# Performance work log

Measured on AMD Instinct MI355X. Metric: run time of the kernel, lower is better.

Reference implementation:

```python
import jax, jax.numpy as jnp
import numpy as np

N_NODES = 65536
N_EDGES = 524288
N_GRAPHS = 512
G_NODES = 10000
NUM_DISEASES = 2000
IN_DIM = 128
HID = 256  # 2 * IN_DIM (z_emb concat feat)
D_FEAT = 512
C_FEAT = 512
MAX_Z = 4000


def setup_inputs() -> dict:
    key = jax.random.key(0)
    ks = jax.random.split(key, 20)
    rn = lambda k, shape: jax.random.normal(k, shape, dtype=jnp.float32) * 0.05
    return {
        "z": jax.random.randint(ks[0], (N_NODES,), 0, MAX_Z),
        "node_id": jnp.sort(jax.random.randint(ks[1], (N_NODES,), 0, G_NODES)),
        "src": jax.random.randint(ks[2], (N_EDGES,), 0, N_NODES),
        "dst": jax.random.randint(ks[3], (N_EDGES,), 0, N_NODES),
        "graph_ids": jnp.sort(jax.random.randint(ks[4], (N_NODES,), 0, N_GRAPHS)),
        "z_table": rn(ks[5], (MAX_Z, IN_DIM)),
        "d_feat_tab": rn(ks[6], (G_NODES, D_FEAT)),
        "c_feat_tab": rn(ks[7], (G_NODES, C_FEAT)),
        "Wd": rn(ks[8], (D_FEAT, IN_DIM)),
        "Wc": rn(ks[9], (C_FEAT, IN_DIM)),
        "gin_W1": rn(ks[10], (HID, HID)), "gin_b1": jnp.zeros((HID,), jnp.float32),
        "gin_W2": rn(ks[11], (HID, HID)), "gin_b2": jnp.zeros((HID,), jnp.float32),
        "sage_Wself": rn(ks[12], (HID, HID)),
        "sage_Wneigh": rn(ks[13], (HID, HID)),
        "sage_b": jnp.zeros((HID,), jnp.float32),
        "lin1_W": rn(ks[14], (HID, HID)), "lin1_b": jnp.zeros((HID,), jnp.float32),
        "lin2_W": rn(ks[15], (HID, 1)), "lin2_b": jnp.zeros((1,), jnp.float32),
    }


def reference(z, node_id, src, dst, graph_ids, z_table, d_feat_tab, c_feat_tab,
              Wd, Wc, gin_W1, gin_b1, gin_W2, gin_b2,
              sage_Wself, sage_Wneigh, sage_b, lin1_W, lin1_b, lin2_W, lin2_b):
    # --- input feature construction (Model.forward) ---
    z_emb = z_table[z]                               # [N, IN_DIM]
    d_proj = d_feat_tab[node_id] @ Wd                # d_fc (bias=False)
    c_proj = c_feat_tab[node_id] @ Wc                # c_fc (bias=False)
    disease = (node_id <= NUM_DISEASES)[:, None]
    # node_id is sorted -> masked concat order == node order
    feat = jnp.where(disease, d_proj, c_proj)        # [N, IN_DIM]
    x = jnp.concatenate([z_emb, feat], axis=1)       # [N, HID]
    # --- GINConv: sum aggregation, eps=0, mlp = Lin->ReLU->Lin ---
    agg = jax.ops.segment_sum(x[src], dst, num_segments=N_NODES)
    h = x + agg
    h = jax.nn.relu(h @ gin_W1 + gin_b1) @ gin_W2 + gin_b2
    # --- SAGEConv('mean'): fc_self(h) + fc_neigh(mean_neighbors) + bias ---
    deg = jax.ops.segment_sum(jnp.ones((N_EDGES,), h.dtype), dst, num_segments=N_NODES)
    mean_n = jax.ops.segment_sum(h[src], dst, num_segments=N_NODES) / jnp.maximum(deg, 1.0)[:, None]
    h = h @ sage_Wself + mean_n @ sage_Wneigh + sage_b
    # --- per-graph max pooling readout ---
    g = jax.ops.segment_max(h, graph_ids, num_segments=N_GRAPHS, indices_are_sorted=True)
    g = jnp.where(jnp.isfinite(g), g, 0.0)           # guard empty graphs
    # --- head: Linear -> ReLU -> (dropout p=0, eval) -> Linear ---
    h = jax.nn.relu(g @ lin1_W + lin1_b)
    return h @ lin2_W + lin2_b                       # [N_GRAPHS, 1]
```

## Files before the change

kernel.cpp:

```cpp
#include <hip/hip_runtime.h>
#include <hip/hip_bf16.h>

#define N_NODES     65536
#define N_EDGES     524288
#define N_GRAPHS    512
#define G_NODES_N   10000
#define NUM_DIS     2000
#define IN_DIM      128
#define HID         256
#define D_FEAT      512
#define MAX_Z       4000

typedef _Float16 half8 __attribute__((ext_vector_type(8)));
typedef float    f32x4 __attribute__((ext_vector_type(4)));

typedef __attribute__((address_space(1))) const void as1_void;
typedef __attribute__((address_space(3))) void       as3_void;

__global__ __launch_bounds__(256) void prep_kernel(
    const float* __restrict__ Ws, const float* __restrict__ Wn,
    const float* __restrict__ Wd, const float* __restrict__ Wc,
    const float* __restrict__ W1, const float* __restrict__ W2,
    const float* __restrict__ z_table,
    const int* __restrict__ z, const int* __restrict__ node_id,
    _Float16* __restrict__ WsT, _Float16* __restrict__ WnT,
    _Float16* __restrict__ WdT, _Float16* __restrict__ WcT,
    _Float16* __restrict__ W12P, _Float16* __restrict__ zt16,
    int2* __restrict__ zn2, int* __restrict__ cnt, int* __restrict__ flags)
{
    const int b = blockIdx.x;
    const int tid = threadIdx.x;
    if (b < 64) {
        __shared__ float tile[64][65];
        const float* W; _Float16* T; int K, N, k0, n0;
        if (b < 32) {
            const int mat = b >> 4, t = b & 15;
            K = HID; N = HID; k0 = (t >> 2) * 64; n0 = (t & 3) * 64;
            W = (mat == 0) ? Ws : Wn;
            T = (mat == 0) ? WsT : WnT;
        } else {
            const int bb = b - 32;
            const int mat = bb >> 4, t = bb & 15;
            K = D_FEAT; N = IN_DIM; k0 = (t >> 1) * 64; n0 = (t & 1) * 64;
            W = (mat == 0) ? Wd : Wc;
            T = (mat == 0) ? WdT : WcT;
        }
        const int tx = tid & 63, ty = tid >> 6;
        #pragma unroll
        for (int r = 0; r < 64; r += 4)
            tile[r + ty][tx] = W[(size_t)(k0 + r + ty) * N + n0 + tx];
        __syncthreads();
        #pragma unroll
        for (int c = 0; c < 64; c += 4)
            T[(size_t)(n0 + c + ty) * K + k0 + tx] = (_Float16)tile[tx][c + ty];
    } else if (b < 576) {
        const int bb = b - 64;
        const int mat = bb >> 8;
        const int k = bb & 255;
        const int n = tid;
        const float* W = mat ? W2 : W1;
        const float v = W[(size_t)k * HID + n];
        const size_t idx = (size_t)(mat * 8 + (k >> 5)) * 8192
                         + (size_t)((((k >> 3) & 3) * 256 + n) * 8 + (k & 7));
        W12P[idx] = (_Float16)v;
    } else if (b < 826) {
        const size_t base = ((size_t)(b - 576) * 256 + tid) * 8;
        const float4 f0 = *(const float4*)(z_table + base);
        const float4 f1 = *(const float4*)(z_table + base + 4);
        half8 h;
        h[0]=(_Float16)f0.x; h[1]=(_Float16)f0.y; h[2]=(_Float16)f0.z; h[3]=(_Float16)f0.w;
        h[4]=(_Float16)f1.x; h[5]=(_Float16)f1.y; h[6]=(_Float16)f1.z; h[7]=(_Float16)f1.w;
        *(half8*)(zt16 + base) = h;
    } else if (b < 890) {
        const int base = (b - 826) * 1024 + tid * 4;
        *(int4*)(cnt + base) = make_int4(0, 0, 0, 0);
        if (b == 826 && tid < 128) flags[tid] = 0;
    } else {
        const int i = (b - 890) * 256 + tid;
        zn2[i] = make_int2(z[i], node_id[i]);
    }
}

__global__ __launch_bounds__(256) void proj_hist_kernel(
    const float* __restrict__ dtab, const float* __restrict__ ctab,
    const _Float16* __restrict__ WdT, const _Float16* __restrict__ WcT,
    _Float16* __restrict__ proj,
    const int* __restrict__ dst, int* __restrict__ cnt)
{
    const int blk = blockIdx.x;
    if (blk >= 79) {
        const int e = (blk - 79) * 256 + threadIdx.x;
        if (e < N_EDGES) atomicAdd(&cnt[dst[e]], 1);
        return;
    }
    __shared__ _Float16 Alds[128 * 40];
    __shared__ _Float16 Blds[128 * 40];
    const float* tab; const _Float16* WT; int base, M, bm;
    if (blk < 16) { tab = dtab; WT = WdT; base = 0;           M = NUM_DIS + 1;             bm = blk * 128; }
    else          { tab = ctab; WT = WcT; base = NUM_DIS + 1; M = G_NODES_N - NUM_DIS - 1; bm = (blk - 16) * 128; }
    const int tid  = threadIdx.x;
    const int wave = tid >> 6, lane = tid & 63;
    const int q    = lane >> 4, l16 = lane & 15;
    const int mbase = (wave & 1) * 64, nbase = (wave >> 1) * 64;
    const int r = tid >> 1, s = tid & 1;

    f32x4 acc[4][4] = {};

    for (int kc = 0; kc < 16; ++kc) {
        const int k0 = kc * 32;
        const int arow = min(bm + r, M - 1);
        const float* gA = tab + (size_t)(base + arow) * D_FEAT + k0 + s * 16;
        const _Float16* gB = WT + (size_t)r * D_FEAT + k0 + s * 16;
        const float4 f0 = ((const float4*)gA)[0];
        const float4 f1 = ((const float4*)gA)[1];
        const float4 f2 = ((const float4*)gA)[2];
        const float4 f3 = ((const float4*)gA)[3];
        const half8 hb0 = *(const half8*)gB;
        const half8 hb1 = *(const half8*)(gB + 8);
        half8 h0, h1;
        h0[0]=(_Float16)f0.x; h0[1]=(_Float16)f0.y; h0[2]=(_Float16)f0.z; h0[3]=(_Float16)f0.w;
        h0[4]=(_Float16)f1.x; h0[5]=(_Float16)f1.y; h0[6]=(_Float16)f1.z; h0[7]=(_Float16)f1.w;
        h1[0]=(_Float16)f2.x; h1[1]=(_Float16)f2.y; h1[2]=(_Float16)f2.z; h1[3]=(_Float16)f2.w;
        h1[4]=(_Float16)f3.x; h1[5]=(_Float16)f3.y; h1[6]=(_Float16)f3.z; h1[7]=(_Float16)f3.w;
        __syncthreads();
        *(half8*)&Alds[r * 40 + s * 16]     = h0;
        *(half8*)&Alds[r * 40 + s * 16 + 8] = h1;
        *(half8*)&Blds[r * 40 + s * 16]     = hb0;
        *(half8*)&Blds[r * 40 + s * 16 + 8] = hb1;
        __syncthreads();
        half8 a[4], b[4];
        #pragma unroll
        for (int i = 0; i < 4; ++i)
            a[i] = *(const half8*)&Alds[(mbase + i * 16 + l16) * 40 + q * 8];
        #pragma unroll
        for (int j = 0; j < 4; ++j)
            b[j] = *(const half8*)&Blds[(nbase + j * 16 + l16) * 40 + q * 8];
        #pragma unroll
        for (int i = 0; i < 4; ++i)
            #pragma unroll
            for (int j = 0; j < 4; ++j)
                acc[i][j] = __builtin_amdgcn_mfma_f32_16x16x32_f16(a[i], b[j], acc[i][j], 0, 0, 0);
    }

    #pragma unroll
    for (int j = 0; j < 4; ++j) {
        const int colg = nbase + j * 16 + l16;
        #pragma unroll
        for (int i = 0; i < 4; ++i) {
            #pragma unroll
            for (int rr = 0; rr < 4; ++rr) {
                const int row = bm + mbase + i * 16 + q * 4 + rr;
                if (row < M)
                    proj[(size_t)(base + row) * IN_DIM + colg] = (_Float16)acc[i][j][rr];
            }
        }
    }
}

__global__ __launch_bounds__(256) void scan_fused_kernel(
    const int* __restrict__ cnt, int* __restrict__ row_ptr,
    int* __restrict__ fill, int* __restrict__ flags)
{
    __shared__ int a[256], b[256];
    __shared__ int sums[64];
    __shared__ int segbase;
    const int t = threadIdx.x;
    const int blk = blockIdx.x;
    const int base = blk * 1024 + t * 4;
    const int4 c = *(const int4*)(cnt + base);
    const int s = c.x + c.y + c.z + c.w;
    a[t] = s;
    __syncthreads();
    int* in = a; int* out = b;
    for (int off = 1; off < 256; off <<= 1) {
        out[t] = in[t] + ((t >= off) ? in[t - off] : 0);
        __syncthreads();
        int* tmp = in; in = out; out = tmp;
    }
    if (t == 0) {
        atomicExch(&flags[64 + blk], in[255]);
        __threadfence();
        atomicAdd(&flags[0], 1);
        while (atomicAdd(&flags[0], 0) < 64) {}
    }
    __syncthreads();
    if (t < 64) sums[t] = atomicAdd(&flags[64 + t], 0);
    __syncthreads();
    if (t == 0) {
        int pfx = 0;
        for (int i = 0; i < blk; ++i) pfx += sums[i];
        segbase = pfx;
        if (blk == 63) {
            int tot = pfx;
            for (int i = blk; i < 64; ++i) tot += sums[i];
            row_ptr[N_NODES] = tot;
        }
    }
    __syncthreads();
    const int run = in[t] - s + segbase;
    int4 r;
    r.x = run; r.y = run + c.x; r.z = r.y + c.y; r.w = r.z + c.z;
    *(int4*)(row_ptr + base) = r;
    *(int4*)(fill + base) = r;
}

__global__ __launch_bounds__(256) void scatter_kernel(
    const int* __restrict__ src, const int* __restrict__ dst,
    const int2* __restrict__ zn2,
    int* __restrict__ fill, int* __restrict__ col, int2* __restrict__ colzn)
{
    const int e = blockIdx.x * 256 + threadIdx.x;
    if (e < N_EDGES) {
        const int s = src[e];
        const int pos = atomicAdd(&fill[dst[e]], 1);
        col[pos] = s;
        colzn[pos] = zn2[s];
    }
}

__global__ __launch_bounds__(256) void gin_fused_kernel(
    const int* __restrict__ row_ptr, const int2* __restrict__ colzn,
    const int2* __restrict__ zn2,
    const _Float16* __restrict__ zt16, const _Float16* __restrict__ proj,
    const _Float16* __restrict__ W12P,
    const float* __restrict__ b1, const float* __restrict__ b2,
    _Float16* __restrict__ H)
{
    __shared__ _Float16 Apanel[64 * 264];
    __shared__ _Float16 Blds[8192];

    const int bm   = blockIdx.x * 64;
    const int tid  = threadIdx.x;
    const int wave = tid >> 6, lane = tid & 63;
    const int q    = lane >> 4, l16 = lane & 15;
    const int nbase = wave * 64;
    const int sb   = wave * 256 + lane;

    {
        #pragma unroll
        for (int tt = 0; tt < 4; ++tt) {
            const int seg = (wave * 4 + tt) * 64 + lane;
            __builtin_amdgcn_global_load_lds((as1_void*)(W12P + seg * 8),
                (as3_void*)&Blds[(wave * 4 + tt) * 64 * 8], 16, 0, 0);
        }
    }

    {
        const int p = tid & 7;
        #pragma unroll 1
        for (int pass = 0; pass < 2; ++pass) {
            const int r  = (tid >> 3) + (pass << 5);
            const int gr = bm + r;
            const int beg = row_ptr[gr], end = row_ptr[gr + 1];
            float za[16], pa[16];
            {
                const int2 zn = zn2[gr];
                const half8* zp = (const half8*)(zt16 + (size_t)zn.x * IN_DIM + p * 16);
                const half8* pp = (const half8*)(proj + (size_t)zn.y * IN_DIM + p * 16);
                const half8 z0 = zp[0], z1 = zp[1], p0 = pp[0], p1 = pp[1];
                #pragma unroll
                for (int i = 0; i < 8; ++i) {
                    za[i] = (float)z0[i]; za[8 + i] = (float)z1[i];
                    pa[i] = (float)p0[i]; pa[8 + i] = (float)p1[i];
                }
            }
            int e = beg;
            for (; e + 4 <= end; e += 4) {
                const int2 znA = colzn[e],     znB = colzn[e + 1];
                const int2 znC = colzn[e + 2], znD = colzn[e + 3];
                const half8* zpA = (const half8*)(zt16 + (size_t)znA.x * IN_DIM + p * 16);
                const half8* ppA = (const half8*)(proj + (size_t)znA.y * IN_DIM + p * 16);
                const half8* zpB = (const half8*)(zt16 + (size_t)znB.x * IN_DIM + p * 16);
                const half8* ppB = (const half8*)(proj + (size_t)znB.y * IN_DIM + p * 16);
                const half8* zpC = (const half8*)(zt16 + (size_t)znC.x * IN_DIM + p * 16);
                const half8* ppC = (const half8*)(proj + (size_t)znC.y * IN_DIM + p * 16);
                const half8* zpD = (const half8*)(zt16 + (size_t)znD.x * IN_DIM + p * 16);
                const half8* ppD = (const half8*)(proj + (size_t)znD.y * IN_DIM + p * 16);
                const half8 zA0 = zpA[0], zA1 = zpA[1], pA0 = ppA[0], pA1 = ppA[1];
                const half8 zB0 = zpB[0], zB1 = zpB[1], pB0 = ppB[0], pB1 = ppB[1];
                const half8 zC0 = zpC[0], zC1 = zpC[1], pC0 = ppC[0], pC1 = ppC[1];
                const half8 zD0 = zpD[0], zD1 = zpD[1], pD0 = ppD[0], pD1 = ppD[1];
                #pragma unroll
                for (int i = 0; i < 8; ++i) {
                    za[i]     += ((float)zA0[i] + (float)zB0[i]) + ((float)zC0[i] + (float)zD0[i]);
                    za[8 + i] += ((float)zA1[i] + (float)zB1[i]) + ((float)zC1[i] + (float)zD1[i]);
                    pa[i]     += ((float)pA0[i] + (float)pB0[i]) + ((float)pC0[i] + (float)pD0[i]);
                    pa[8 + i] += ((float)pA1[i] + (float)pB1[i]) + ((float)pC1[i] + (float)pD1[i]);
                }
            }
            for (; e + 2 <= end; e += 2) {
                const int2 znA = colzn[e];
                const int2 znB = colzn[e + 1];
                const half8* zpA = (const half8*)(zt16 + (size_t)znA.x * IN_DIM + p * 16);
                const half8* ppA = (const half8*)(proj + (size_t)znA.y * IN_DIM + p * 16);
                const half8* zpB = (const half8*)(zt16 + (size_t)znB.x * IN_DIM + p * 16);
                const half8* ppB = (const half8*)(proj + (size_t)znB.y * IN_DIM + p * 16);
                const half8 zA0 = zpA[0], zA1 = zpA[1], pA0 = ppA[0], pA1 = ppA[1];
                const half8 zB0 = zpB[0], zB1 = zpB[1], pB0 = ppB[0], pB1 = ppB[1];
                #pragma unroll
                for (int i = 0; i < 8; ++i) {
                    za[i]     += (float)zA0[i] + (float)zB0[i];
                    za[8 + i] += (float)zA1[i] + (float)zB1[i];
                    pa[i]     += (float)pA0[i] + (float)pB0[i];
                    pa[8 + i] += (float)pA1[i] + (float)pB1[i];
                }
            }
            if (e < end) {
                const int2 zn = colzn[e];
                const half8* zp = (const half8*)(zt16 + (size_t)zn.x * IN_DIM + p * 16);
                const half8* pp = (const half8*)(proj + (size_t)zn.y * IN_DIM + p * 16);
                const half8 z0 = zp[0], z1 = zp[1], p0 = pp[0], p1 = pp[1];
                #pragma unroll
                for (int i = 0; i < 8; ++i) {
                    za[i] += (float)z0[i]; za[8 + i] += (float)z1[i];
                    pa[i] += (float)p0[i]; pa[8 + i] += (float)p1[i];
                }
            }
            half8 oz0, oz1, op0, op1;
            #pragma unroll
            for (int i = 0; i < 8; ++i) {
                oz0[i] = (_Float16)za[i];     oz1[i] = (_Float16)za[8 + i];
                op0[i] = (_Float16)pa[i];     op1[i] = (_Float16)pa[8 + i];
            }
            *(half8*)&Apanel[r * 264 + p * 16]           = oz0;
            *(half8*)&Apanel[r * 264 + p * 16 + 8]       = oz1;
            *(half8*)&Apanel[r * 264 + 128 + p * 16]     = op0;
            *(half8*)&Apanel[r * 264 + 128 + p * 16 + 8] = op1;
        }
    }
    __syncthreads();

    half8 pf0, pf1, pf2, pf3;
    auto pfetch = [&](int c) {
        const _Float16* s = W12P + (size_t)c * 8192 + (size_t)sb * 8;
        pf0 = *(const half8*)(s);
        pf1 = *(const half8*)(s + 512);
        pf2 = *(const half8*)(s + 1024);
        pf3 = *(const half8*)(s + 1536);
    };
    pfetch(1);

    f32x4 acc[4][4] = {};
    for (int c = 0; c < 16; ++c) {
        const int kl = (c & 7) * 32;
        half8 a[4], b[4];
        #pragma unroll
        for (int i = 0; i < 4; ++i)
            a[i] = *(const half8*)&Apanel[(i * 16 + l16) * 264 + kl + q * 8];
        #pragma unroll
        for (int j = 0; j < 4; ++j)
            b[j] = *(const half8*)&Blds[(q * 256 + nbase + j * 16 + l16) * 8];
        #pragma unroll
        for (int i = 0; i < 4; ++i)
            #pragma unroll
            for (int j = 0; j < 4; ++j)
                acc[i][j] = __builtin_amdgcn_mfma_f32_16x16x32_f16(a[i], b[j], acc[i][j], 0, 0, 0);
        if (c == 15) break;
        __syncthreads();
        *(half8*)&Blds[sb * 8]         = pf0;
        *(half8*)&Blds[(sb + 64) * 8]  = pf1;
        *(half8*)&Blds[(sb + 128) * 8] = pf2;
        *(half8*)&Blds[(sb + 192) * 8] = pf3;
        if (c == 7) {
            #pragma unroll
            for (int j = 0; j < 4; ++j) {
                const int colg = nbase + j * 16 + l16;
                const float bv = b1[colg];
                #pragma unroll
                for (int i = 0; i < 4; ++i)
                    #pragma unroll
                    for (int rr = 0; rr < 4; ++rr) {
                        const float v = fmaxf(acc[i][j][rr] + bv, 0.0f);
                        Apanel[(i * 16 + q * 4 + rr) * 264 + colg] = (_Float16)v;
                        acc[i][j][rr] = 0.0f;
                    }
            }
        }
        if (c < 14) pfetch(c + 2);
        __syncthreads();
    }

    #pragma unroll
    for (int j = 0; j < 4; ++j) {
        const int colg = nbase + j * 16 + l16;
        const float bv = b2[colg];
        #pragma unroll
        for (int i = 0; i < 4; ++i)
            #pragma unroll
            for (int rr = 0; rr < 4; ++rr) {
                const int rowg = bm + i * 16 + q * 4 + rr;
                H[(size_t)rowg * HID + colg] = (_Float16)(acc[i][j][rr] + bv);
            }
    }
}

__global__ __launch_bounds__(256) void csr_agg_kernel(
    const int* __restrict__ row_ptr, const int* __restrict__ col,
    const _Float16* __restrict__ F, _Float16* __restrict__ OUT)
{
    const int t = blockIdx.x * 256 + threadIdx.x;
    const int d = t >> 5;
    const int q = t & 31;
    const int beg = row_ptr[d];
    const int end = row_ptr[d + 1];
    float acc[8] = {0.f,0.f,0.f,0.f,0.f,0.f,0.f,0.f};
    int e = beg;
    for (; e + 8 <= end; e += 8) {
        const int s0 = col[e],     s1 = col[e + 1];
        const int s2 = col[e + 2], s3 = col[e + 3];
        const int s4 = col[e + 4], s5 = col[e + 5];
        const int s6 = col[e + 6], s7 = col[e + 7];
        const half8 v0 = *(const half8*)(F + (size_t)s0 * HID + q * 8);
        const half8 v1 = *(const half8*)(F + (size_t)s1 * HID + q * 8);
        const half8 v2 = *(const half8*)(F + (size_t)s2 * HID + q * 8);
        const half8 v3 = *(const half8*)(F + (size_t)s3 * HID + q * 8);
        const half8 v4 = *(const half8*)(F + (size_t)s4 * HID + q * 8);
        const half8 v5 = *(const half8*)(F + (size_t)s5 * HID + q * 8);
        const half8 v6 = *(const half8*)(F + (size_t)s6 * HID + q * 8);
        const half8 v7 = *(const half8*)(F + (size_t)s7 * HID + q * 8);
        #pragma unroll
        for (int i = 0; i < 8; ++i)
            acc[i] += (((float)v0[i] + (float)v1[i]) + ((float)v2[i] + (float)v3[i]))
                    + (((float)v4[i] + (float)v5[i]) + ((float)v6[i] + (float)v7[i]));
    }
    for (; e + 4 <= end; e += 4) {
        const int s0 = col[e],     s1 = col[e + 1];
        const int s2 = col[e + 2], s3 = col[e + 3];
        const half8 v0 = *(const half8*)(F + (size_t)s0 * HID + q * 8);
        const half8 v1 = *(const half8*)(F + (size_t)s1 * HID + q * 8);
        const half8 v2 = *(const half8*)(F + (size_t)s2 * HID + q * 8);
        const half8 v3 = *(const half8*)(F + (size_t)s3 * HID + q * 8);
        #pragma unroll
        for (int i = 0; i < 8; ++i)
            acc[i] += ((float)v0[i] + (float)v1[i]) + ((float)v2[i] + (float)v3[i]);
    }
    for (; e < end; ++e) {
        const half8 v0 = *(const half8*)(F + (size_t)col[e] * HID + q * 8);
        #pragma unroll
        for (int i = 0; i < 8; ++i) acc[i] += (float)v0[i];
    }
    const float rs = 1.0f / fmaxf((float)(end - beg), 1.0f);
    half8 o;
    #pragma unroll
    for (int i = 0; i < 8; ++i) o[i] = (_Float16)(acc[i] * rs);
    *(half8*)(OUT + (size_t)d * HID + q * 8) = o;
}

__global__ __launch_bounds__(256) void mfma_gemm_kernel(
    const _Float16* __restrict__ A1, const _Float16* __restrict__ A2,
    const _Float16* __restrict__ B1T, const _Float16* __restrict__ B2T,
    const float* __restrict__ bias, _Float16* __restrict__ Ch)
{
    __shared__ _Float16 Alds[128 * 32];
    __shared__ _Float16 Blds[128 * 32];
    const int bm   = blockIdx.x * 128;
    const int bn   = blockIdx.y * 128;
    const int tid  = threadIdx.x;
    const int wave = tid >> 6, lane = tid & 63;
    const int q    = lane >> 4, l16 = lane & 15;
    const int mbase = (wave & 1) * 64, nbase = (wave >> 1) * 64;

    const int i0 = wave * 128 + lane;
    const int i1 = i0 + 64;
    const int r0 = i0 >> 2, s0 = i0 & 3;
    const int r1 = i1 >> 2, s1 = i1 & 3;

    half8 pa0, pa1, pb0, pb1;
    auto pfetch = [&](int kc) {
        const int k0 = (kc & 7) * 32;
        const _Float16* Ab = (kc < 8) ? A1 : A2;
        const _Float16* Bb = (kc < 8) ? B1T : B2T;
        pa0 = *(const half8*)(Ab + (size_t)(bm + r0) * HID + k0 + s0 * 8);
        pa1 = *(const half8*)(Ab + (size_t)(bm + r1) * HID + k0 + s1 * 8);
        pb0 = *(const half8*)(Bb + (size_t)(bn + r0) * HID + k0 + s0 * 8);
        pb1 = *(const half8*)(Bb + (size_t)(bn + r1) * HID + k0 + s1 * 8);
    };
    pfetch(0);

    f32x4 acc[4][4] = {};

    for (int kc = 0; kc < 16; ++kc) {
        __syncthreads();
        *(half8*)&Alds[i0 * 8] = pa0;
        *(half8*)&Alds[i1 * 8] = pa1;
        *(half8*)&Blds[i0 * 8] = pb0;
        *(half8*)&Blds[i1 * 8] = pb1;
        if (kc < 15) pfetch(kc + 1);
        __syncthreads();
        half8 a[4], b[4];
        #pragma unroll
        for (int i = 0; i < 4; ++i)
            a[i] = *(const half8*)&Alds[(mbase + i * 16 + l16) * 32 + q * 8];
        #pragma unroll
        for (int j = 0; j < 4; ++j)
            b[j] = *(const half8*)&Blds[(nbase + j * 16 + l16) * 32 + q * 8];
        #pragma unroll
        for (int i = 0; i < 4; ++i)
            #pragma unroll
            for (int j = 0; j < 4; ++j)
                acc[i][j] = __builtin_amdgcn_mfma_f32_16x16x32_f16(a[i], b[j], acc[i][j], 0, 0, 0);
    }

    #pragma unroll
    for (int j = 0; j < 4; ++j) {
        const int colg = bn + nbase + j * 16 + l16;
        const float bv = bias[colg];
        #pragma unroll
        for (int i = 0; i < 4; ++i) {
            #pragma unroll
            for (int rr = 0; rr < 4; ++rr) {
                const int rowg = bm + mbase + i * 16 + q * 4 + rr;
                Ch[(size_t)rowg * HID + colg] = (_Float16)(acc[i][j][rr] + bv);
            }
        }
    }
}

__global__ __launch_bounds__(256) void pool_head_kernel(
    const _Float16* __restrict__ H2, const int* __restrict__ gid,
    const float* __restrict__ W1, const float* __restrict__ b1,
    const float* __restrict__ W2, const float* __restrict__ b2,
    float* __restrict__ out)
{
    const int g = blockIdx.x;
    const int tid = threadIdx.x;
    int lo = 0, hi = N_NODES;
    while (lo < hi) { const int mid = (lo + hi) >> 1; if (gid[mid] < g) lo = mid + 1; else hi = mid; }
    const int start = lo;
    hi = N_NODES;
    while (lo < hi) { const int mid = (lo + hi) >> 1; if (gid[mid] < g + 1) lo = mid + 1; else hi = mid; }
    const int end = lo;

    const int rowofs = tid >> 5;
    const int q = tid & 31;
    float m8[8];
    #pragma unroll
    for (int k = 0; k < 8; ++k) m8[k] = -INFINITY;
    for (int i = start + rowofs; i < end; i += 8) {
        const half8 v = *(const half8*)(H2 + (size_t)i * HID + q * 8);
        #pragma unroll
        for (int k = 0; k < 8; ++k) m8[k] = fmaxf(m8[k], (float)v[k]);
    }
    __shared__ float part[8][256];
    #pragma unroll
    for (int k = 0; k < 8; ++k) part[rowofs][q * 8 + k] = m8[k];
    __syncthreads();
    __shared__ float row[HID];
    __shared__ float red[HID];
    const int j = tid;
    float m = part[0][j];
    #pragma unroll
    for (int r = 1; r < 8; ++r) m = fmaxf(m, part[r][j]);
    row[j] = (m == -INFINITY) ? 0.0f : m;
    __syncthreads();
    float acc = b1[j];
    #pragma unroll 8
    for (int k = 0; k < HID; ++k)
        acc = fmaf(row[k], W1[k * HID + j], acc);
    acc = fmaxf(acc, 0.f);
    red[j] = acc * W2[j];
    __syncthreads();
    for (int s = 128; s > 0; s >>= 1) {
        if (j < s) red[j] += red[j + s];
        __syncthreads();
    }
    if (j == 0) out[g] = red[0] + b2[0];
}

extern "C" void kernel_launch(void* const* d_in, const int* in_sizes, int n_in,
                              void* d_out, int out_size, void* d_ws, size_t ws_size,
                              hipStream_t stream)
{
    const int*   z         = (const int*)d_in[0];
    const int*   node_id   = (const int*)d_in[1];
    const int*   src       = (const int*)d_in[2];
    const int*   dst       = (const int*)d_in[3];
    const int*   graph_ids = (const int*)d_in[4];
    const float* z_table   = (const float*)d_in[5];
    const float* d_feat    = (const float*)d_in[6];
    const float* c_feat    = (const float*)d_in[7];
    const float* Wd        = (const float*)d_in[8];
    const float* Wc        = (const float*)d_in[9];
    const float* gin_W1    = (const float*)d_in[10];
    const float* gin_b1    = (const float*)d_in[11];
    const float* gin_W2    = (const float*)d_in[12];
    const float* gin_b2    = (const float*)d_in[13];
    const float* sage_Wself  = (const float*)d_in[14];
    const float* sage_Wneigh = (const float*)d_in[15];
    const float* sage_b    = (const float*)d_in[16];
    const float* lin1_W    = (const float*)d_in[17];
    const float* lin1_b    = (const float*)d_in[18];
    const float* lin2_W    = (const float*)d_in[19];
    const float* lin2_b    = (const float*)d_in[20];
    float* out = (float*)d_out;

    const size_t NH = (size_t)N_NODES * HID;
    char* wsb = (char*)d_ws;
    _Float16* Hh   = (_Float16*)wsb;                     wsb += NH * 2;
    _Float16* AGGh = (_Float16*)wsb;                     wsb += NH * 2;
    _Float16* H2h  = (_Float16*)wsb;                     wsb += NH * 2;
    _Float16* projh= (_Float16*)wsb;                     wsb += (size_t)G_NODES_N * IN_DIM * 2;
    _Float16* W12P = (_Float16*)wsb;                     wsb += 16 * 8192 * 2;
    _Float16* WsT  = (_Float16*)wsb;                     wsb += HID * HID * 2;
    _Float16* WnT  = (_Float16*)wsb;                     wsb += HID * HID * 2;
    _Float16* WdT  = (_Float16*)wsb;                     wsb += D_FEAT * IN_DIM * 2;
    _Float16* WcT  = (_Float16*)wsb;                     wsb += D_FEAT * IN_DIM * 2;
    _Float16* zt16 = (_Float16*)wsb;                     wsb += (size_t)MAX_Z * IN_DIM * 2;
    int2* zn2      = (int2*)wsb;                         wsb += (size_t)N_NODES * 8;
    int2* colzn    = (int2*)wsb;                         wsb += (size_t)N_EDGES * 8;
    int* row_ptr   = (int*)wsb;                          wsb += (N_NODES + 4) * 4;
    int* cnt       = (int*)wsb;                          wsb += N_NODES * 4;
    int* fill      = (int*)wsb;                          wsb += N_NODES * 4;
    int* col       = (int*)wsb;                          wsb += N_EDGES * 4;
    int* flags     = (int*)wsb;                          wsb += 128 * 4;

    prep_kernel<<<1146, 256, 0, stream>>>(
        sage_Wself, sage_Wneigh, Wd, Wc, gin_W1, gin_W2, z_table, z, node_id,
        WsT, WnT, WdT, WcT, W12P, zt16, zn2, cnt, flags);

    proj_hist_kernel<<<79 + N_EDGES / 256, 256, 0, stream>>>(
        d_feat, c_feat, WdT, WcT, projh, dst, cnt);

    scan_fused_kernel<<<64, 256, 0, stream>>>(cnt, row_ptr, fill, flags);
    scatter_kernel<<<N_EDGES / 256, 256, 0, stream>>>(src, dst, zn2, fill, col, colzn);

    gin_fused_kernel<<<N_NODES / 64, 256, 0, stream>>>(
        row_ptr, colzn, zn2, zt16, projh, W12P, gin_b1, gin_b2, Hh);

    csr_agg_kernel<<<(N_NODES * 32) / 256, 256, 0, stream>>>(row_ptr, col, Hh, AGGh);

    dim3 ggrid(N_NODES / 128, HID / 128);
    mfma_gemm_kernel<<<ggrid, 256, 0, stream>>>(Hh, AGGh, WsT, WnT, sage_b, H2h);

    pool_head_kernel<<<N_GRAPHS, 256, 0, stream>>>(
        H2h, graph_ids, lin1_W, lin1_b, lin2_W, lin2_b, out);
}
```

Baseline: 343.9 us.

## Use 512-thread blocks in fused GIN kernel with pre-scaled byte offsets

The fused GIN kernel now launches 512 threads per block, so each thread gathers one row instead of two sequential passes. The 8 waves are arranged as a 2x4 grid over the 64x256 output tile, which halves each wave's MFMA accumulator footprint. zn2 indices are pre-shifted to byte offsets to drop address multiplies, and the next four edge indices are software-prefetched. Occupancy may drop because of the larger block, and the colzn buffer is padded to cover the prefetch.

```diff
diff --git a/kernel.cpp b/kernel.cpp
--- a/kernel.cpp
+++ b/kernel.cpp
@@ -77,7 +77,7 @@
         if (b == 826 && tid < 128) flags[tid] = 0;
     } else {
         const int i = (b - 890) * 256 + tid;
-        zn2[i] = make_int2(z[i], node_id[i]);
+        zn2[i] = make_int2(z[i] << 8, node_id[i] << 8);
     }
 }
 
@@ -218,7 +218,7 @@
     }
 }
 
-__global__ __launch_bounds__(256) void gin_fused_kernel(
+__global__ __launch_bounds__(512) void gin_fused_kernel(
     const int* __restrict__ row_ptr, const int2* __restrict__ colzn,
     const int2* __restrict__ zn2,
     const _Float16* __restrict__ zt16, const _Float16* __restrict__ proj,
@@ -233,145 +233,146 @@
     const int tid  = threadIdx.x;
     const int wave = tid >> 6, lane = tid & 63;
     const int q    = lane >> 4, l16 = lane & 15;
-    const int nbase = wave * 64;
-    const int sb   = wave * 256 + lane;
-
-    {
-        #pragma unroll
-        for (int tt = 0; tt < 4; ++tt) {
-            const int seg = (wave * 4 + tt) * 64 + lane;
-            __builtin_amdgcn_global_load_lds((as1_void*)(W12P + seg * 8),
-                (as3_void*)&Blds[(wave * 4 + tt) * 64 * 8], 16, 0, 0);
-        }
+    const int wr   = wave >> 2;
+    const int wc   = wave & 3;
+    const int rbase = wr * 32;
+    const int nbase = wc * 64;
+
+    #pragma unroll
+    for (int tt = 0; tt < 2; ++tt) {
+        const int seg = (wave * 2 + tt) * 64 + lane;
+        __builtin_amdgcn_global_load_lds((as1_void*)(W12P + seg * 8),
+            (as3_void*)&Blds[(wave * 2 + tt) * 64 * 8], 16, 0, 0);
     }
 
     {
         const int p = tid & 7;
-        #pragma unroll 1
-        for (int pass = 0; pass < 2; ++pass) {
-            const int r  = (tid >> 3) + (pass << 5);
-            const int gr = bm + r;
-            const int beg = row_ptr[gr], end = row_ptr[gr + 1];
-            float za[16], pa[16];
-            {
-                const int2 zn = zn2[gr];
-                const half8* zp = (const half8*)(zt16 + (size_t)zn.x * IN_DIM + p * 16);
-                const half8* pp = (const half8*)(proj + (size_t)zn.y * IN_DIM + p * 16);
-                const half8 z0 = zp[0], z1 = zp[1], p0 = pp[0], p1 = pp[1];
-                #pragma unroll
-                for (int i = 0; i < 8; ++i) {
-                    za[i] = (float)z0[i]; za[8 + i] = (float)z1[i];
-                    pa[i] = (float)p0[i]; pa[8 + i] = (float)p1[i];
-                }
-            }
-            int e = beg;
-            for (; e + 4 <= end; e += 4) {
-                const int2 znA = colzn[e],     znB = colzn[e + 1];
-                const int2 znC = colzn[e + 2], znD = colzn[e + 3];
-                const half8* zpA = (const half8*)(zt16 + (size_t)znA.x * IN_DIM + p * 16);
-                const half8* ppA = (const half8*)(proj + (size_t)znA.y * IN_DIM + p * 16);
-                const half8* zpB = (const half8*)(zt16 + (size_t)znB.x * IN_DIM + p * 16);
-                const half8* ppB = (const half8*)(proj + (size_t)znB.y * IN_DIM + p * 16);
-                const half8* zpC = (const half8*)(zt16 + (size_t)znC.x * IN_DIM + p * 16);
-                const half8* ppC = (const half8*)(proj + (size_t)znC.y * IN_DIM + p * 16);
-                const half8* zpD = (const half8*)(zt16 + (size_t)znD.x * IN_DIM + p * 16);
-                const half8* ppD = (const half8*)(proj + (size_t)znD.y * IN_DIM + p * 16);
-                const half8 zA0 = zpA[0], zA1 = zpA[1], pA0 = ppA[0], pA1 = ppA[1];
-                const half8 zB0 = zpB[0], zB1 = zpB[1], pB0 = ppB[0], pB1 = ppB[1];
-                const half8 zC0 = zpC[0], zC1 = zpC[1], pC0 = ppC[0], pC1 = ppC[1];
-                const half8 zD0 = zpD[0], zD1 = zpD[1], pD0 = ppD[0], pD1 = ppD[1];
-                #pragma unroll
-                for (int i = 0; i < 8; ++i) {
-                    za[i]     += ((float)zA0[i] + (float)zB0[i]) + ((float)zC0[i] + (float)zD0[i]);
-                    za[8 + i] += ((float)zA1[i] + (float)zB1[i]) + ((float)zC1[i] + (float)zD1[i]);
-                    pa[i]     += ((float)pA0[i] + (float)pB0[i]) + ((float)pC0[i] + (float)pD0[i]);
-                    pa[8 + i] += ((float)pA1[i] + (float)pB1[i]) + ((float)pC1[i] + (float)pD1[i]);
-                }
-            }
-            for (; e + 2 <= end; e += 2) {
-                const int2 znA = colzn[e];
-                const int2 znB = colzn[e + 1];
-                const half8* zpA = (const half8*)(zt16 + (size_t)znA.x * IN_DIM + p * 16);
-                const half8* ppA = (const half8*)(proj + (size_t)znA.y * IN_DIM + p * 16);
-                const half8* zpB = (const half8*)(zt16 + (size_t)znB.x * IN_DIM + p * 16);
-                const half8* ppB = (const half8*)(proj + (size_t)znB.y * IN_DIM + p * 16);
-                const half8 zA0 = zpA[0], zA1 = zpA[1], pA0 = ppA[0], pA1 = ppA[1];
-                const half8 zB0 = zpB[0], zB1 = zpB[1], pB0 = ppB[0], pB1 = ppB[1];
-                #pragma unroll
-                for (int i = 0; i < 8; ++i) {
-                    za[i]     += (float)zA0[i] + (float)zB0[i];
-                    za[8 + i] += (float)zA1[i] + (float)zB1[i];
-                    pa[i]     += (float)pA0[i] + (float)pB0[i];
-                    pa[8 + i] += (float)pA1[i] + (float)pB1[i];
-                }
-            }
-            if (e < end) {
-                const int2 zn = colzn[e];
-                const half8* zp = (const half8*)(zt16 + (size_t)zn.x * IN_DIM + p * 16);
-                const half8* pp = (const half8*)(proj + (size_t)zn.y * IN_DIM + p * 16);
-                const half8 z0 = zp[0], z1 = zp[1], p0 = pp[0], p1 = pp[1];
-                #pragma unroll
-                for (int i = 0; i < 8; ++i) {
-                    za[i] += (float)z0[i]; za[8 + i] += (float)z1[i];
-                    pa[i] += (float)p0[i]; pa[8 + i] += (float)p1[i];
-                }
-            }
-            half8 oz0, oz1, op0, op1;
+        const int r = tid >> 3;
+        const int gr = bm + r;
+        const int beg = row_ptr[gr], end = row_ptr[gr + 1];
+        const char* ztb = (const char*)zt16 + p * 32;
+        const char* prb = (const char*)proj + p * 32;
+        float za[16], pa[16];
+        {
+            const int2 zn = zn2[gr];
+            const half8* zp = (const half8*)(ztb + zn.x);
+            const half8* pp = (const half8*)(prb + zn.y);
+            const half8 z0 = zp[0], z1 = zp[1], p0 = pp[0], p1 = pp[1];
             #pragma unroll
             for (int i = 0; i < 8; ++i) {
-                oz0[i] = (_Float16)za[i];     oz1[i] = (_Float16)za[8 + i];
-                op0[i] = (_Float16)pa[i];     op1[i] = (_Float16)pa[8 + i];
-            }
-            *(half8*)&Apanel[r * 264 + p * 16]           = oz0;
-            *(half8*)&Apanel[r * 264 + p * 16 + 8]       = oz1;
-            *(half8*)&Apanel[r * 264 + 128 + p * 16]     = op0;
-            *(half8*)&Apanel[r * 264 + 128 + p * 16 + 8] = op1;
-        }
-    }
-    __syncthreads();
-
-    half8 pf0, pf1, pf2, pf3;
+                za[i] = (float)z0[i]; za[8 + i] = (float)z1[i];
+                pa[i] = (float)p0[i]; pa[8 + i] = (float)p1[i];
+            }
+        }
+        int e = beg;
+        int2 iA, iB, iC, iD;
+        if (e + 4 <= end) {
+            iA = colzn[e]; iB = colzn[e + 1]; iC = colzn[e + 2]; iD = colzn[e + 3];
+        }
+        for (; e + 4 <= end; e += 4) {
+            const half8* zpA = (const half8*)(ztb + iA.x);
+            const half8* ppA = (const half8*)(prb + iA.y);
+            const half8* zpB = (const half8*)(ztb + iB.x);
+            const half8* ppB = (const half8*)(prb + iB.y);
+            const half8* zpC = (const half8*)(ztb + iC.x);
+            const half8* ppC = (const half8*)(prb + iC.y);
+            const half8* zpD = (const half8*)(ztb + iD.x);
+            const half8* ppD = (const half8*)(prb + iD.y);
+            const half8 zA0 = zpA[0], zA1 = zpA[1], pA0 = ppA[0], pA1 = ppA[1];
+            const half8 zB0 = zpB[0], zB1 = zpB[1], pB0 = ppB[0], pB1 = ppB[1];
+            const half8 zC0 = zpC[0], zC1 = zpC[1], pC0 = ppC[0], pC1 = ppC[1];
+            const half8 zD0 = zpD[0], zD1 = zpD[1], pD0 = ppD[0], pD1 = ppD[1];
+            if (e + 8 <= end) {
+                iA = colzn[e + 4]; iB = colzn[e + 5];
+                iC = colzn[e + 6]; iD = colzn[e + 7];
+            }
+            #pragma unroll
+            for (int i = 0; i < 8; ++i) {
+                za[i]     += ((float)zA0[i] + (float)zB0[i]) + ((float)zC0[i] + (float)zD0[i]);
+                za[8 + i] += ((float)zA1[i] + (float)zB1[i]) + ((float)zC1[i] + (float)zD1[i]);
+                pa[i]     += ((float)pA0[i] + (float)pB0[i]) + ((float)pC0[i] + (float)pD0[i]);
+                pa[8 + i] += ((float)pA1[i] + (float)pB1[i]) + ((float)pC1[i] + (float)pD1[i]);
+            }
+        }
+        for (; e + 2 <= end; e += 2) {
+            const int2 jA = colzn[e];
+            const int2 jB = colzn[e + 1];
+            const half8* zpA = (const half8*)(ztb + jA.x);
+            const half8* ppA = (const half8*)(prb + jA.y);
+            const half8* zpB = (const half8*)(ztb + jB.x);
+            const half8* ppB = (const half8*)(prb + jB.y);
+            const half8 zA0 = zpA[0], zA1 = zpA[1], pA0 = ppA[0], pA1 = ppA[1];
+            const half8 zB0 = zpB[0], zB1 = zpB[1], pB0 = ppB[0], pB1 = ppB[1];
+            #pragma unroll
+            for (int i = 0; i < 8; ++i) {
+                za[i]     += (float)zA0[i] + (float)zB0[i];
+                za[8 + i] += (float)zA1[i] + (float)zB1[i];
+                pa[i]     += (float)pA0[i] + (float)pB0[i];
+                pa[8 + i] += (float)pA1[i] + (float)pB1[i];
+            }
+        }
+        if (e < end) {
+            const int2 jA = colzn[e];
+            const half8* zp = (const half8*)(ztb + jA.x);
+            const half8* pp = (const half8*)(prb + jA.y);
+            const half8 z0 = zp[0], z1 = zp[1], p0 = pp[0], p1 = pp[1];
+            #pragma unroll
+            for (int i = 0; i < 8; ++i) {
+                za[i] += (float)z0[i]; za[8 + i] += (float)z1[i];
+                pa[i] += (float)p0[i]; pa[8 + i] += (float)p1[i];
+            }
+        }
+        half8 oz0, oz1, op0, op1;
+        #pragma unroll
+        for (int i = 0; i < 8; ++i) {
+            oz0[i] = (_Float16)za[i];     oz1[i] = (_Float16)za[8 + i];
+            op0[i] = (_Float16)pa[i];     op1[i] = (_Float16)pa[8 + i];
+        }
+        *(half8*)&Apanel[r * 264 + p * 16]           = oz0;
+        *(half8*)&Apanel[r * 264 + p * 16 + 8]       = oz1;
+        *(half8*)&Apanel[r * 264 + 128 + p * 16]     = op0;
+        *(half8*)&Apanel[r * 264 + 128 + p * 16 + 8] = op1;
+    }
+    __syncthreads();
+
+    half8 pf0, pf1;
     auto pfetch = [&](int c) {
-        const _Float16* s = W12P + (size_t)c * 8192 + (size_t)sb * 8;
+        const _Float16* s = W12P + (size_t)c * 8192 + (size_t)tid * 8;
         pf0 = *(const half8*)(s);
-        pf1 = *(const half8*)(s + 512);
-        pf2 = *(const half8*)(s + 1024);
-        pf3 = *(const half8*)(s + 1536);
+        pf1 = *(const half8*)(s + 4096);
     };
     pfetch(1);
 
-    f32x4 acc[4][4] = {};
+    f32x4 acc[2][4] = {};
     for (int c = 0; c < 16; ++c) {
         const int kl = (c & 7) * 32;
-        half8 a[4], b[4];
-        #pragma unroll
-        for (int i = 0; i < 4; ++i)
-            a[i] = *(const half8*)&Apanel[(i * 16 + l16) * 264 + kl + q * 8];
+        half8 a[2], b[4];
+        #pragma unroll
+        for (int i = 0; i < 2; ++i)
+            a[i] = *(const half8*)&Apanel[(rbase + i * 16 + l16) * 264 + kl + q * 8];
         #pragma unroll
         for (int j = 0; j < 4; ++j)
             b[j] = *(const half8*)&Blds[(q * 256 + nbase + j * 16 + l16) * 8];
         #pragma unroll
-        for (int i = 0; i < 4; ++i)
+        for (int i = 0; i < 2; ++i)
             #pragma unroll
             for (int j = 0; j < 4; ++j)
                 acc[i][j] = __builtin_amdgcn_mfma_f32_16x16x32_f16(a[i], b[j], acc[i][j], 0, 0, 0);
         if (c == 15) break;
         __syncthreads();
-        *(half8*)&Blds[sb * 8]         = pf0;
-        *(half8*)&Blds[(sb + 64) * 8]  = pf1;
-        *(half8*)&Blds[(sb + 128) * 8] = pf2;
-        *(half8*)&Blds[(sb + 192) * 8] = pf3;
+        *(half8*)&Blds[tid * 8]         = pf0;
+        *(half8*)&Blds[(tid + 512) * 8] = pf1;
         if (c == 7) {
             #pragma unroll
             for (int j = 0; j < 4; ++j) {
                 const int colg = nbase + j * 16 + l16;
                 const float bv = b1[colg];
                 #pragma unroll
-                for (int i = 0; i < 4; ++i)
+                for (int i = 0; i < 2; ++i)
                     #pragma unroll
                     for (int rr = 0; rr < 4; ++rr) {
                         const float v = fmaxf(acc[i][j][rr] + bv, 0.0f);
-                        Apanel[(i * 16 + q * 4 + rr) * 264 + colg] = (_Float16)v;
+                        Apanel[(rbase + i * 16 + q * 4 + rr) * 264 + colg] = (_Float16)v;
                         acc[i][j][rr] = 0.0f;
                     }
             }
@@ -385,10 +386,10 @@
         const int colg = nbase + j * 16 + l16;
         const float bv = b2[colg];
         #pragma unroll
-        for (int i = 0; i < 4; ++i)
+        for (int i = 0; i < 2; ++i)
             #pragma unroll
             for (int rr = 0; rr < 4; ++rr) {
-                const int rowg = bm + i * 16 + q * 4 + rr;
+                const int rowg = bm + rbase + i * 16 + q * 4 + rr;
                 H[(size_t)rowg * HID + colg] = (_Float16)(acc[i][j][rr] + bv);
             }
     }
@@ -607,7 +608,7 @@
     _Float16* WcT  = (_Float16*)wsb;                     wsb += D_FEAT * IN_DIM * 2;
     _Float16* zt16 = (_Float16*)wsb;                     wsb += (size_t)MAX_Z * IN_DIM * 2;
     int2* zn2      = (int2*)wsb;                         wsb += (size_t)N_NODES * 8;
-    int2* colzn    = (int2*)wsb;                         wsb += (size_t)N_EDGES * 8;
+    int2* colzn    = (int2*)wsb;                         wsb += (size_t)(N_EDGES + 8) * 8;
     int* row_ptr   = (int*)wsb;                          wsb += (N_NODES + 4) * 4;
     int* cnt       = (int*)wsb;                          wsb += N_NODES * 4;
     int* fill      = (int*)wsb;                          wsb += N_NODES * 4;
@@ -624,7 +625,7 @@
     scan_fused_kernel<<<64, 256, 0, stream>>>(cnt, row_ptr, fill, flags);
     scatter_kernel<<<N_EDGES / 256, 256, 0, stream>>>(src, dst, zn2, fill, col, colzn);
 
-    gin_fused_kernel<<<N_NODES / 64, 256, 0, stream>>>(
+    gin_fused_kernel<<<N_NODES / 64, 512, 0, stream>>>(
         row_ptr, colzn, zn2, zt16, projh, W12P, gin_b1, gin_b2, Hh);
 
     csr_agg_kernel<<<(N_NODES * 32) / 256, 256, 0, stream>>>(row_ptr, col, Hh, AGGh);
```

After: 345.4 us. About the same (+0.4%).
